# Optimization experiments

Measured on AMD Instinct MI355X. Metric: run time of the kernel, lower is better.

Reference implementation:

```python
import jax, jax.numpy as jnp
import numpy as np

N_SLOTS, BATCH, READ = 512, 1024, 128

def setup_inputs() -> dict:
    key = jax.random.key(0)
    ks = jax.random.split(key, 7)
    values = jax.random.normal(ks[0], (N_SLOTS, BATCH, READ), jnp.float32)  # stored memory slots
    S = jax.random.uniform(ks[1], (N_SLOTS, BATCH, 1), jnp.float32)         # per-slot strengths (>=0)
    u = jax.random.uniform(ks[2], (BATCH, 1), jnp.float32) * 4.0            # total pop strength
    d1 = jax.random.uniform(ks[3], (BATCH, 1), jnp.float32)
    d2 = jax.random.uniform(ks[4], (BATCH, 1), jnp.float32)
    v1 = jax.random.normal(ks[5], (BATCH, READ), jnp.float32)
    v2 = jax.random.normal(ks[6], (BATCH, READ), jnp.float32)
    return {"values": values, "S": S, "u": u, "d1": d1, "d2": d2, "v1": v1, "v2": v2}

def reference(values, S, u, d1, d2, v1, v2):
    # push(d1, d2, v1, v2): append two (strength, value) pairs to the memory.
    vals = jnp.concatenate([values, v1[None], v2[None]], axis=0)   # [N+2, B, R]
    stren = jnp.concatenate([S, d1[None], d2[None]], axis=0)       # [N+2, B, 1]
    # pop(u): stack (LIFO) read order = newest slot first.
    # The sequential loop   per_used_i = min(S_i, max(u - strength_used, 0))
    # with strength_used accumulating per_used is equivalent (by induction:
    # strength_used = min(cumsum(S), u)) to a clipped exclusive prefix sum:
    s_rev = stren[::-1]                                            # [N+2, B, 1]
    v_rev = vals[::-1]                                             # [N+2, B, R]
    cum_prev = jnp.cumsum(s_rev, axis=0) - s_rev                   # exclusive prefix sum of strengths
    per_used = jnp.minimum(s_rev, jnp.maximum(u[None] - cum_prev, 0.0))  # [N+2, B, 1]
    # summary = sum_i values_i * per_used_i  (weighted read)
    summary = jnp.einsum('nbr,nb->br', v_rev, per_used[..., 0])    # [B, R]
    return summary
```

## Files before the change

### kernel.cpp

```cpp
#include <hip/hip_runtime.h>

#define N_SLOTS 512
#define BATCH   1024
#define READ    128
#define N_TOT   (N_SLOTS + 2)

__global__ __launch_bounds__(128) void nm_summary_kernel(
    const float* __restrict__ values,
    const float* __restrict__ S,
    const float* __restrict__ u,
    const float* __restrict__ d1,
    const float* __restrict__ d2,
    const float* __restrict__ v1,
    const float* __restrict__ v2,
    float* __restrict__ out)
{
    const int b   = blockIdx.x;
    const int tid = threadIdx.x;

    __shared__ float w_lds[N_TOT];
    __shared__ int   n_used_s;

    const float ub = u[b];

    if (tid < 64) {
        const int lane = tid;
        float carry = 0.0f;
        int   last  = 0;

        for (int c = 0; c < N_TOT; c += 64) {
            const int i = c + lane;
            float s = 0.0f;
            if (i < N_TOT) {
                s = (i == 0) ? d2[b]
                  : (i == 1) ? d1[b]
                  : S[(size_t)(513 - i) * BATCH + b];
            }
            float x = s;
            #pragma unroll
            for (int off = 1; off < 64; off <<= 1) {
                float t = __shfl_up(x, off, 64);
                if (lane >= off) x += t;
            }
            const float cum_prev = carry + x - s;
            const float w = fminf(s, fmaxf(ub - cum_prev, 0.0f));
            if (i < N_TOT) w_lds[i] = w;

            const unsigned long long m = __ballot(w > 0.0f);
            if (m) last = c + (63 - __builtin_clzll(m)) + 1;

            carry += __shfl(x, 63, 64);
            if (carry >= ub) break;
        }
        if (lane == 0) n_used_s = last;
    }
    __syncthreads();

    const int n_used = n_used_s;
    const int r = tid;
    float acc = 0.0f;
    for (int n = 0; n < n_used; ++n) {
        const float w = w_lds[n];
        const float* src;
        if (n == 0)      src = v2 + (size_t)b * READ;
        else if (n == 1) src = v1 + (size_t)b * READ;
        else             src = values + ((size_t)(513 - n) * BATCH + b) * READ;
        acc = fmaf(src[r], w, acc);
    }
    out[(size_t)b * READ + r] = acc;
}

extern "C" void kernel_launch(void* const* d_in, const int* in_sizes, int n_in,
                              void* d_out, int out_size, void* d_ws, size_t ws_size,
                              hipStream_t stream) {
    const float* values = (const float*)d_in[0];
    const float* S      = (const float*)d_in[1];
    const float* u      = (const float*)d_in[2];
    const float* d1     = (const float*)d_in[3];
    const float* d2     = (const float*)d_in[4];
    const float* v1     = (const float*)d_in[5];
    const float* v2     = (const float*)d_in[6];
    float* out = (float*)d_out;

    nm_summary_kernel<<<dim3(BATCH), dim3(128), 0, stream>>>(
        values, S, u, d1, d2, v1, v2, out);
}
```

Baseline: 9.826 us.

## Prefetch first value rows before the strength scan and use one wave per batch

The block shrinks to a single 64-lane wave, and each lane handles two read columns through float2 loads. The first 16 value rows are loaded into registers before the prefix-sum scan, so their memory latency overlaps with the S loads and the scan instead of waiting behind them. The weighted sum uses those prefetched rows unconditionally and then loops over any remaining used slots. The cost is extra register pressure and reading up to 16 rows even when fewer slots carry weight, since the mean slot strength of 0.5 against u up to 4 means only about 8 rows are typically needed.

```diff
diff --git a/kernel.cpp b/kernel.cpp
--- a/kernel.cpp
+++ b/kernel.cpp
@@ -3,9 +3,10 @@
 #define N_SLOTS 512
 #define BATCH   1024
 #define READ    128
-#define N_TOT   (N_SLOTS + 2)
+#define N_TOT   514
+#define PF      16
 
-__global__ __launch_bounds__(128) void nm_summary_kernel(
+__global__ __launch_bounds__(64) void nm_summary_kernel(
     const float* __restrict__ values,
     const float* __restrict__ S,
     const float* __restrict__ u,
@@ -15,59 +16,77 @@
     const float* __restrict__ v2,
     float* __restrict__ out)
 {
-    const int b   = blockIdx.x;
-    const int tid = threadIdx.x;
+    const int b    = blockIdx.x;
+    const int lane = threadIdx.x;
 
     __shared__ float w_lds[N_TOT];
-    __shared__ int   n_used_s;
 
     const float ub = u[b];
+    float s = (lane == 0) ? d2[b]
+            : (lane == 1) ? d1[b]
+            : S[(size_t)(513 - lane) * BATCH + b];
 
-    if (tid < 64) {
-        const int lane = tid;
-        float carry = 0.0f;
-        int   last  = 0;
+    float2 pf[PF];
+    pf[0] = ((const float2*)(v2 + (size_t)b * READ))[lane];
+    pf[1] = ((const float2*)(v1 + (size_t)b * READ))[lane];
+    #pragma unroll
+    for (int n = 2; n < PF; ++n) {
+        const float2* row =
+            (const float2*)(values + ((size_t)(513 - n) * BATCH + b) * (size_t)READ);
+        pf[n] = row[lane];
+    }
 
-        for (int c = 0; c < N_TOT; c += 64) {
-            const int i = c + lane;
-            float s = 0.0f;
-            if (i < N_TOT) {
-                s = (i == 0) ? d2[b]
-                  : (i == 1) ? d1[b]
-                  : S[(size_t)(513 - i) * BATCH + b];
-            }
-            float x = s;
-            #pragma unroll
-            for (int off = 1; off < 64; off <<= 1) {
-                float t = __shfl_up(x, off, 64);
-                if (lane >= off) x += t;
-            }
-            const float cum_prev = carry + x - s;
-            const float w = fminf(s, fmaxf(ub - cum_prev, 0.0f));
-            if (i < N_TOT) w_lds[i] = w;
-
-            const unsigned long long m = __ballot(w > 0.0f);
-            if (m) last = c + (63 - __builtin_clzll(m)) + 1;
-
-            carry += __shfl(x, 63, 64);
-            if (carry >= ub) break;
+    float carry = 0.0f;
+    int   n_used = 0;
+    {
+        float x = s;
+        #pragma unroll
+        for (int off = 1; off < 64; off <<= 1) {
+            float t = __shfl_up(x, off, 64);
+            if (lane >= off) x += t;
         }
-        if (lane == 0) n_used_s = last;
+        const float cum_prev = x - s;
+        const float w = fminf(s, fmaxf(ub - cum_prev, 0.0f));
+        w_lds[lane] = w;
+        const unsigned long long m = __ballot(w > 0.0f);
+        if (m) n_used = (63 - __builtin_clzll(m)) + 1;
+        carry = __shfl(x, 63, 64);
+    }
+    for (int c = 64; c < N_TOT && carry < ub; c += 64) {
+        const int i = c + lane;
+        float s2 = (i < N_TOT) ? S[(size_t)(513 - i) * BATCH + b] : 0.0f;
+        float x = s2;
+        #pragma unroll
+        for (int off = 1; off < 64; off <<= 1) {
+            float t = __shfl_up(x, off, 64);
+            if (lane >= off) x += t;
+        }
+        const float cum_prev = carry + x - s2;
+        const float w = fminf(s2, fmaxf(ub - cum_prev, 0.0f));
+        if (i < N_TOT) w_lds[i] = w;
+        const unsigned long long m = __ballot(w > 0.0f);
+        if (m) n_used = c + (63 - __builtin_clzll(m)) + 1;
+        carry += __shfl(x, 63, 64);
     }
     __syncthreads();
 
-    const int n_used = n_used_s;
-    const int r = tid;
-    float acc = 0.0f;
-    for (int n = 0; n < n_used; ++n) {
+    float2 acc = make_float2(0.0f, 0.0f);
+    #pragma unroll
+    for (int n = 0; n < PF; ++n) {
         const float w = w_lds[n];
-        const float* src;
-        if (n == 0)      src = v2 + (size_t)b * READ;
-        else if (n == 1) src = v1 + (size_t)b * READ;
-        else             src = values + ((size_t)(513 - n) * BATCH + b) * READ;
-        acc = fmaf(src[r], w, acc);
+        acc.x = fmaf(pf[n].x, w, acc.x);
+        acc.y = fmaf(pf[n].y, w, acc.y);
     }
-    out[(size_t)b * READ + r] = acc;
+    for (int n = PF; n < n_used; ++n) {
+        const float w = w_lds[n];
+        const float2* row =
+            (const float2*)(values + ((size_t)(513 - n) * BATCH + b) * (size_t)READ);
+        const float2 v = row[lane];
+        acc.x = fmaf(v.x, w, acc.x);
+        acc.y = fmaf(v.y, w, acc.y);
+    }
+
+    ((float2*)(out + (size_t)b * READ))[lane] = acc;
 }
 
 extern "C" void kernel_launch(void* const* d_in, const int* in_sizes, int n_in,
@@ -82,6 +101,6 @@
     const float* v2     = (const float*)d_in[6];
     float* out = (float*)d_out;
 
-    nm_summary_kernel<<<dim3(BATCH), dim3(128), 0, stream>>>(
+    nm_summary_kernel<<<dim3(BATCH), dim3(64), 0, stream>>>(
         values, S, u, d1, d2, v1, v2, out);
 }
```

Result: no change. 9.737 us (median of 2 runs) (-0.9%).
